# Kernel optimization log

Measured on AMD Instinct MI355X. Metric: run time of the kernel, lower is better.

Reference implementation:

```python
import jax, jax.numpy as jnp
import numpy as np

EPS_LN = 1e-5

def _layernorm(x, g, b):
    mu = x.mean(-1, keepdims=True)
    var = ((x - mu) ** 2).mean(-1, keepdims=True)
    return (x - mu) / jnp.sqrt(var + EPS_LN) * g + b


def setup_inputs() -> dict:
    key = jax.random.key(0)
    B, N, D, H = 4, 2048, 256, 4
    hid = int(D * 2.0)
    ks = jax.random.split(key, 12)
    x = jax.random.normal(ks[0], (B, N, D), jnp.float32)
    Au = jax.random.uniform(ks[1], (N, N)) < 0.004
    A = jnp.logical_or(Au, Au.T)
    A = A.at[jnp.arange(N), jnp.arange(N)].set(False)
    Af = A.astype(jnp.float32)
    deg = Af.sum(axis=1)
    L = jnp.diag(deg) - Af                      # graph Laplacian (N,N), PSD
    adjacency = Af + jnp.eye(N, dtype=jnp.float32)  # self loops so no empty softmax rows
    s = lambda k, sh, f: jax.random.normal(k, sh, jnp.float32) * f
    sc = 1.0 / np.sqrt(D)
    Wc = s(ks[2], (D, D), sc); bc = jnp.zeros((D,), jnp.float32)
    Wq = s(ks[3], (D, D), sc); Wk = s(ks[4], (D, D), sc); Wv = s(ks[5], (D, D), sc)
    Wo = s(ks[6], (D, D), sc); bo = jnp.zeros((D,), jnp.float32)
    W1 = s(ks[7], (D, hid), sc); b1 = jnp.zeros((hid,), jnp.float32)
    W2 = s(ks[8], (hid, D), 1.0 / np.sqrt(hid)); b2 = jnp.zeros((D,), jnp.float32)
    g1 = jnp.ones((D,), jnp.float32); be1 = jnp.zeros((D,), jnp.float32)
    g2 = jnp.ones((D,), jnp.float32); be2 = jnp.zeros((D,), jnp.float32)
    g3 = jnp.ones((D,), jnp.float32); be3 = jnp.zeros((D,), jnp.float32)
    return dict(x=x, L=L, adjacency=adjacency, Wc=Wc, bc=bc, g1=g1, be1=be1,
                Wq=Wq, Wk=Wk, Wv=Wv, Wo=Wo, bo=bo, g2=g2, be2=be2,
                W1=W1, b1=b1, W2=W2, b2=b2, g3=g3, be3=be3)


def reference(x, L, adjacency, Wc, bc, g1, be1, Wq, Wk, Wv, Wo, bo,
              g2, be2, W1, b1, W2, b2, g3, be3):
    B, N, D = x.shape
    H = 4
    hd = D // H
    # --- LaplacianConv: normalize L to eigenvalues in [-1, 1] ---
    eig = jnp.linalg.eigvalsh(L)               # ascending
    lam_max = eig[-1] + 1e-8
    L_norm = 2.0 * L / lam_max - jnp.eye(N, dtype=L.dtype)
    # per-channel matmul in torch == single propagation L_norm @ x
    xp = jnp.einsum('mn,bnf->bmf', L_norm, x)
    h = xp @ Wc + bc
    h = _layernorm(h, g1, be1)
    h = jax.nn.relu(h)
    x1 = h + x                                  # residual (in_dim == out_dim)
    # --- adjacency-masked multi-head attention ---
    q = (x1 @ Wq).reshape(B, N, H, hd).transpose(0, 2, 1, 3)  # (B,H,N,hd)
    k = (x1 @ Wk).reshape(B, N, H, hd).transpose(0, 2, 1, 3)
    v = (x1 @ Wv).reshape(B, N, H, hd).transpose(0, 2, 1, 3)
    scores = jnp.einsum('bhnd,bhmd->bhnm', q, k) / np.sqrt(hd).astype(np.float32)
    scores = jnp.where(adjacency[None, None] > 0, scores, jnp.float32(-1e9))
    attn = jax.nn.softmax(scores, axis=-1)
    o = jnp.einsum('bhnm,bhmd->bhnd', attn, v)
    o = o.transpose(0, 2, 1, 3).reshape(B, N, D)
    o = o @ Wo + bo
    x2 = _layernorm(x1 + o, g2, be2)
    # --- MLP ---
    m = jax.nn.gelu(x2 @ W1 + b1, approximate=False) @ W2 + b2
    return _layernorm(x2 + m, g3, be3)
```

## Files before the change

### kernel.cpp

```cpp
#include <hip/hip_runtime.h>
#include <math.h>

typedef __bf16 bf16;
typedef bf16 bf16x8 __attribute__((ext_vector_type(8)));
typedef float f32x4 __attribute__((ext_vector_type(4)));

#define LDS_PAD 40
#define SENT 2048
#define LANCZOS_M 14

__global__ __launch_bounds__(256) void k_pre(
    const float* __restrict__ Wc, const float* __restrict__ Wq, const float* __restrict__ Wk,
    const float* __restrict__ Wv, const float* __restrict__ Wo, const float* __restrict__ W1,
    const float* __restrict__ W2, const float* __restrict__ x, const float* __restrict__ adj,
    bf16* __restrict__ WcT, bf16* __restrict__ WqT, bf16* __restrict__ WkT,
    bf16* __restrict__ WvT, bf16* __restrict__ WoT, bf16* __restrict__ W1T,
    bf16* __restrict__ W2T, bf16* __restrict__ xT,
    int* __restrict__ cnt, unsigned short* __restrict__ cols,
    const float* __restrict__ L, bf16* __restrict__ Lb)
{
    __shared__ float tile[32][33];
    int z = blockIdx.z;
    if (z == 11) {
        int flat = blockIdx.y * 16 + blockIdx.x;
        if (flat >= 512) return;
        int row = flat * 4 + (threadIdx.x >> 6);
        int lane = threadIdx.x & 63;
        int base = 0;
        for (int c0 = 0; c0 < 2048; c0 += 64) {
            float a = adj[(long)row * 2048 + c0 + lane];
            unsigned long long m = __ballot(a != 0.0f);
            if (a != 0.0f) {
                int pos = base + __popcll(m & ((1ull << lane) - 1ull));
                if (pos < 64) cols[(long)row * 64 + pos] = (unsigned short)(c0 + lane);
            }
            base += __popcll(m);
        }
        int c = base < 64 ? base : 64;
        if (lane >= c) cols[(long)row * 64 + lane] = (unsigned short)SENT;
        if (lane == 0) cnt[row] = c;
        return;
    }
    if (z >= 12) {
        int colBase = (z - 12) * 512 + blockIdx.x * 32;
        int rowBase = blockIdx.y * 32;
        int tx = threadIdx.x & 31, ty = threadIdx.x >> 5;
#pragma unroll
        for (int j = 0; j < 4; ++j) {
            long idx = (long)(rowBase + ty + 8 * j) * 2048 + colBase + tx;
            Lb[idx] = (bf16)L[idx];
        }
        return;
    }
    const float* src; bf16* dst; int R, C;
    switch (z) {
        case 0: src = Wc; dst = WcT; R = 256; C = 256; break;
        case 1: src = Wq; dst = WqT; R = 256; C = 256; break;
        case 2: src = Wk; dst = WkT; R = 256; C = 256; break;
        case 3: src = Wv; dst = WvT; R = 256; C = 256; break;
        case 4: src = Wo; dst = WoT; R = 256; C = 256; break;
        case 5: src = W1; dst = W1T; R = 256; C = 512; break;
        case 6: src = W2; dst = W2T; R = 512; C = 256; break;
        default: {
            int b = z - 7;
            src = x + (long)b * 2048 * 256; dst = xT + (long)b * 256 * 2048;
            R = 2048; C = 256;
        }
    }
    int c0 = blockIdx.x * 32, r0 = blockIdx.y * 32;
    if (c0 >= C || r0 >= R) return;
    int tx = threadIdx.x & 31, ty = threadIdx.x >> 5;
#pragma unroll
    for (int j = 0; j < 4; ++j)
        tile[ty + 8 * j][tx] = src[(long)(r0 + ty + 8 * j) * C + c0 + tx];
    __syncthreads();
#pragma unroll
    for (int j = 0; j < 4; ++j)
        dst[(long)(c0 + ty + 8 * j) * R + r0 + tx] = (bf16)tile[tx][ty + 8 * j];
}

__global__ __launch_bounds__(1024) void k_main(
    const int* __restrict__ cnt, const unsigned short* __restrict__ cols, float* __restrict__ lamOut,
    const bf16* __restrict__ Lb, const bf16* __restrict__ xT, float* __restrict__ xp0f)
{
    __shared__ float va[2064], vb[2064];
    __shared__ float redf[16], redf2[16];
    __shared__ int   redi[16];
    __shared__ float bcast, bcast2;
    __shared__ float alphaA[LANCZOS_M], betaA[LANCZOS_M];
    __shared__ bf16 As[64 * LDS_PAD];
    __shared__ bf16 Bs[256 * LDS_PAD];

    int t = threadIdx.x;
    if (blockIdx.x != 0) {
        int bx = blockIdx.x - 1;
        int rowBlk = (bx & 31) * 64;
        int z  = (bx >> 5) & 3;
        int ks = bx >> 7;
        long kbase = (long)ks * 1024;
        const bf16* BT = xT + (long)z * 256 * 2048;
        int w = t >> 6, lane = t & 63;
        int q = lane >> 4, l15 = lane & 15;
        int wm = w & 3, wn = w >> 2;

        f32x4 acc[4];
#pragma unroll
        for (int i = 0; i < 4; ++i) acc[i] = (f32x4){0.0f, 0.0f, 0.0f, 0.0f};

        int ar = t >> 4, ac = (t & 15) * 2;
        int br = t >> 2, bc = (t & 3) * 8;
        const bf16* Ap = Lb + (long)(rowBlk + ar) * 2048 + kbase + ac;
        const bf16* Bp = BT + (long)br * 2048 + kbase + bc;
        unsigned rA = *(const unsigned*)Ap;
        uint4    rB = *(const uint4*)Bp;
        for (int kt = 0; kt < 1024; kt += 32) {
            __syncthreads();
            *(unsigned*)&As[ar * LDS_PAD + ac] = rA;
            *(uint4*)&Bs[br * LDS_PAD + bc] = rB;
            __syncthreads();
            if (kt + 32 < 1024) {
                rA = *(const unsigned*)(Ap + kt + 32);
                rB = *(const uint4*)(Bp + kt + 32);
            }
            bf16x8 a = *(const bf16x8*)&As[(wm * 16 + l15) * LDS_PAD + q * 8];
#pragma unroll
            for (int nt = 0; nt < 4; ++nt) {
                bf16x8 b = *(const bf16x8*)&Bs[((wn * 4 + nt) * 16 + l15) * LDS_PAD + q * 8];
                acc[nt] = __builtin_amdgcn_mfma_f32_16x16x32_bf16(a, b, acc[nt], 0, 0, 0);
            }
        }
        long zRow = (long)ks * 8192 + (long)z * 2048 + rowBlk + wm * 16 + q * 4;
#pragma unroll
        for (int nt = 0; nt < 4; ++nt) {
            int col = (wn * 4 + nt) * 16 + l15;
#pragma unroll
            for (int r = 0; r < 4; ++r)
                xp0f[(zRow + r) * 256 + col] = acc[nt][r];
        }
        return;
    }
    int wid = t >> 6, lane = t & 63;
    int r0 = t, r1 = t + 1024;
    int c0 = cnt[r0], c1 = cnt[r1];
    int p0 = (c0 + 7) & ~7, p1 = (c1 + 7) & ~7;

    uint4 cr0[8], cr1[8];
#pragma unroll
    for (int j = 0; j < 8; ++j) {
        cr0[j] = ((const uint4*)(cols + (long)r0 * 64))[j];
        cr1[j] = ((const uint4*)(cols + (long)r1 * 64))[j];
    }

    int md = max(c0, c1);
#pragma unroll
    for (int off = 32; off >= 1; off >>= 1) md = max(md, __shfl_xor(md, off));
    if (lane == 0) redi[wid] = md;
    __syncthreads();
    if (t == 0) {
        int m = 0;
        for (int i = 0; i < 16; ++i) m = max(m, redi[i]);
        bcast = (float)(2 * (m - 1)) + 1.0f;
    }
    for (int i = t; i < 2048; i += 1024) {
        unsigned u = (unsigned)i * 2654435761u;
        u ^= u >> 16; u *= 2246822519u; u ^= u >> 13;
        float mag = 0.5f + (float)((u >> 9) & 1023) * (1.0f / 1024.0f);
        va[i] = (u & 1) ? mag : -mag;
    }
    if (t == 0) { va[SENT] = 0.0f; vb[SENT] = 0.0f; }
    __syncthreads();
    float hiBound = bcast;

    float d0 = va[r0], d1 = va[r1];
    float pz = d0 * d0 + d1 * d1;
#pragma unroll
    for (int off = 32; off >= 1; off >>= 1) pz += __shfl_xor(pz, off);
    if (lane == 0) redf[wid] = pz;
    __syncthreads();
    if (t == 0) { float s = 0; for (int i = 0; i < 16; ++i) s += redf[i]; bcast = s; }
    __syncthreads();
    float sc = rsqrtf(fmaxf(bcast, 1e-30f));
    d0 *= sc; d1 *= sc;
    va[r0] = d0; va[r1] = d1;
    __syncthreads();

    float* cur = va; float* nxt = vb;
    float bp = 0.0f;
    float p0r = 0.0f, p1r = 0.0f;
    for (int it = 0; it < LANCZOS_M; ++it) {
        float sum0 = 0.0f, sum1 = 0.0f;
#pragma unroll
        for (int j = 0; j < 8; ++j)
            if (j * 8 < p0) {
                uint4 q = cr0[j];
                sum0 += cur[q.x & 0xffff] + cur[q.x >> 16] + cur[q.y & 0xffff] + cur[q.y >> 16]
                      + cur[q.z & 0xffff] + cur[q.z >> 16] + cur[q.w & 0xffff] + cur[q.w >> 16];
            }
#pragma unroll
        for (int j = 0; j < 8; ++j)
            if (j * 8 < p1) {
                uint4 q = cr1[j];
                sum1 += cur[q.x & 0xffff] + cur[q.x >> 16] + cur[q.y & 0xffff] + cur[q.y >> 16]
                      + cur[q.z & 0xffff] + cur[q.z >> 16] + cur[q.w & 0xffff] + cur[q.w >> 16];
            }
        float u0 = (float)c0 * d0 - sum0 - bp * p0r;
        float u1 = (float)c1 * d1 - sum1 - bp * p1r;
        float puv = u0 * d0 + u1 * d1;
        float puu = u0 * u0 + u1 * u1;
#pragma unroll
        for (int off = 32; off >= 1; off >>= 1) {
            puv += __shfl_xor(puv, off);
            puu += __shfl_xor(puu, off);
        }
        if (lane == 0) { redf[wid] = puv; redf2[wid] = puu; }
        __syncthreads();
        if (t == 0) {
            float sv = 0, su = 0;
            for (int i = 0; i < 16; ++i) { sv += redf[i]; su += redf2[i]; }
            float b = sqrtf(fmaxf(su - sv * sv, 1e-24f));
            alphaA[it] = sv; betaA[it] = b;
            bcast = sv; bcast2 = b;
        }
        __syncthreads();
        float alpha = bcast, beta = bcast2;
        float invb = 1.0f / beta;
        float w0 = u0 - alpha * d0, w1 = u1 - alpha * d1;
        p0r = d0; p1r = d1;
        d0 = w0 * invb; d1 = w1 * invb;
        nxt[r0] = d0; nxt[r1] = d1;
        __syncthreads();
        bp = beta;
        float* tmp = cur; cur = nxt; nxt = tmp;
    }

    if (t < 64) {
        float aa[LANCZOS_M], b2[LANCZOS_M];
#pragma unroll
        for (int i = 0; i < LANCZOS_M; ++i) { aa[i] = alphaA[i]; b2[i] = betaA[i] * betaA[i]; }
        float lo = 0.0f, hi = hiBound;
        for (int round = 0; round < 4; ++round) {
            float step = (hi - lo) * (1.0f / 65.0f);
            float xm = lo + step * (float)(lane + 1);
            float dd = aa[0] - xm;
            int neg = dd < 0.0f ? 1 : 0;
#pragma unroll
            for (int i = 1; i < LANCZOS_M; ++i) {
                float ad = fmaxf(fabsf(dd), 1e-12f);
                dd = (dd < 0.0f) ? -ad : ad;
                dd = aa[i] - xm - b2[i - 1] / dd;
                neg += dd < 0.0f ? 1 : 0;
            }
            unsigned long long mb = __ballot(neg >= LANCZOS_M);
            if (mb == 0ull) {
                lo = lo + step * 64.0f;
            } else {
                int fl = (int)(__ffsll((long long)mb) - 1);
                hi = lo + step * (float)(fl + 1);
                lo = lo + step * (float)fl;
            }
        }
        if (lane == 0) lamOut[0] = 0.5f * (lo + hi) + 1e-8f;
    }
}

template <int TA, int EPI>
__global__ __launch_bounds__(256) void k_gemm(
    const bf16* __restrict__ A0, const float* __restrict__ Apa, const float* __restrict__ Apb,
    const float* __restrict__ Aaux, const bf16* __restrict__ BTg,
    float* __restrict__ outF, bf16* __restrict__ outB,
    const float* __restrict__ bias, const float* __restrict__ resid,
    const float* __restrict__ gam, const float* __restrict__ bet,
    const float* __restrict__ lamPtr,
    int K, long aZ, long btZ, long outZrows, int ldOut)
{
    __shared__ bf16 As[64 * LDS_PAD];
    __shared__ bf16 Bs[256 * LDS_PAD];

    int tid = threadIdx.x;
    int w = tid >> 6, lane = tid & 63;
    int q = lane >> 4, l15 = lane & 15;
    int rowBlk = blockIdx.x * 64;
    int colB = blockIdx.y * 256;
    const bf16* BT = BTg + (long)blockIdx.z * btZ + (long)blockIdx.y * 256 * (long)K;

    float s2 = 0.0f;
    if (TA == 2) s2 = 2.0f / lamPtr[0];

    f32x4 acc[16];
#pragma unroll
    for (int i = 0; i < 16; ++i) acc[i] = (f32x4){0.0f, 0.0f, 0.0f, 0.0f};

    int ar = tid >> 2, ac = (tid & 3) * 8;
    long abase = (long)(rowBlk + ar) * K + ac;
    const bf16* A = A0 + (long)blockIdx.z * aZ;
    const bf16* Bp = BT + (long)tid * K;

    uint4 aR;
    float4 pa0, pa1, pb0, pb1, xa0, xa1;
    uint4 bR0, bR1, bR2, bR3;
    if (TA == 1) {
        aR = *(const uint4*)(A + abase);
    } else {
        pa0 = *(const float4*)(Apa + abase);  pa1 = *(const float4*)(Apa + abase + 4);
        pb0 = *(const float4*)(Apb + abase);  pb1 = *(const float4*)(Apb + abase + 4);
        xa0 = *(const float4*)(Aaux + abase); xa1 = *(const float4*)(Aaux + abase + 4);
    }
    bR0 = ((const uint4*)Bp)[0]; bR1 = ((const uint4*)Bp)[1];
    bR2 = ((const uint4*)Bp)[2]; bR3 = ((const uint4*)Bp)[3];

    for (int kt = 0; kt < K; kt += 32) {
        __syncthreads();
        if (TA == 1) {
            *(uint4*)&As[ar * LDS_PAD + ac] = aR;
        } else {
            float pa[8] = {pa0.x, pa0.y, pa0.z, pa0.w, pa1.x, pa1.y, pa1.z, pa1.w};
            float pb[8] = {pb0.x, pb0.y, pb0.z, pb0.w, pb1.x, pb1.y, pb1.z, pb1.w};
            float xa[8] = {xa0.x, xa0.y, xa0.z, xa0.w, xa1.x, xa1.y, xa1.z, xa1.w};
            union { bf16 h[8]; uint4 u; } pk;
#pragma unroll
            for (int j = 0; j < 8; ++j) pk.h[j] = (bf16)(s2 * (pa[j] + pb[j]) - xa[j]);
            *(uint4*)&As[ar * LDS_PAD + ac] = pk.u;
        }
        {
            bf16* d = &Bs[tid * LDS_PAD];
            *(uint4*)(d + 0)  = bR0;
            *(uint4*)(d + 8)  = bR1;
            *(uint4*)(d + 16) = bR2;
            *(uint4*)(d + 24) = bR3;
        }
        __syncthreads();
        if (kt + 32 < K) {
            long nb = abase + kt + 32;
            if (TA == 1) {
                aR = *(const uint4*)(A + nb);
            } else {
                pa0 = *(const float4*)(Apa + nb);  pa1 = *(const float4*)(Apa + nb + 4);
                pb0 = *(const float4*)(Apb + nb);  pb1 = *(const float4*)(Apb + nb + 4);
                xa0 = *(const float4*)(Aaux + nb); xa1 = *(const float4*)(Aaux + nb + 4);
            }
            const bf16* p = Bp + kt + 32;
            bR0 = ((const uint4*)p)[0]; bR1 = ((const uint4*)p)[1];
            bR2 = ((const uint4*)p)[2]; bR3 = ((const uint4*)p)[3];
        }
        bf16x8 a = *(const bf16x8*)&As[(w * 16 + l15) * LDS_PAD + q * 8];
#pragma unroll
        for (int nt = 0; nt < 16; ++nt) {
            bf16x8 b = *(const bf16x8*)&Bs[(nt * 16 + l15) * LDS_PAD + q * 8];
            acc[nt] = __builtin_amdgcn_mfma_f32_16x16x32_bf16(a, b, acc[nt], 0, 0, 0);
        }
    }

    long zRow = (long)blockIdx.z * outZrows + rowBlk + w * 16 + q * 4;

    if (EPI == 0) {
#pragma unroll
        for (int nt = 0; nt < 16; ++nt) {
            int col = colB + nt * 16 + l15;
#pragma unroll
            for (int r = 0; r < 4; ++r)
                outB[(zRow + r) * (long)ldOut + col] = (bf16)acc[nt][r];
        }
        return;
    }
    if (EPI == 3) {
#pragma unroll
        for (int nt = 0; nt < 16; ++nt) {
            int col = colB + nt * 16 + l15;
            float bi = bias[col];
#pragma unroll
            for (int r = 0; r < 4; ++r) {
                float v = acc[nt][r] + bi;
                float g = 0.5f * v * (1.0f + erff(v * 0.70710678118654752440f));
                outB[(zRow + r) * (long)ldOut + col] = (bf16)g;
            }
        }
        return;
    }
    float s[4] = {0, 0, 0, 0}, sq[4] = {0, 0, 0, 0};
#pragma unroll
    for (int nt = 0; nt < 16; ++nt) {
        int col = colB + nt * 16 + l15;
        float bi = bias[col];
#pragma unroll
        for (int r = 0; r < 4; ++r) {
            float v = acc[nt][r] + bi;
            if (EPI == 2) v += resid[(zRow + r) * 256 + col];
            acc[nt][r] = v;
            s[r] += v; sq[r] += v * v;
        }
    }
#pragma unroll
    for (int off = 1; off <= 8; off <<= 1) {
#pragma unroll
        for (int r = 0; r < 4; ++r) { s[r] += __shfl_xor(s[r], off); sq[r] += __shfl_xor(sq[r], off); }
    }
    float mean[4], rstd[4];
#pragma unroll
    for (int r = 0; r < 4; ++r) {
        mean[r] = s[r] * (1.0f / 256.0f);
        float var = sq[r] * (1.0f / 256.0f) - mean[r] * mean[r];
        rstd[r] = rsqrtf(var + 1e-5f);
    }
#pragma unroll
    for (int nt = 0; nt < 16; ++nt) {
        int col = colB + nt * 16 + l15;
        float gc = gam[col], bc2 = bet[col];
#pragma unroll
        for (int r = 0; r < 4; ++r) {
            float v = (acc[nt][r] - mean[r]) * rstd[r] * gc + bc2;
            if (EPI == 1) v = fmaxf(v, 0.0f) + resid[(zRow + r) * 256 + col];
            long oi = (zRow + r) * (long)ldOut + col;
            outF[oi] = v;
            if (outB) outB[oi] = (bf16)v;
        }
    }
}

__global__ __launch_bounds__(256) void k_attn(const bf16* __restrict__ qg, const bf16* __restrict__ kg,
                                              const bf16* __restrict__ vg, bf16* __restrict__ og,
                                              const int* __restrict__ cnt, const unsigned short* __restrict__ cols)
{
    __shared__ unsigned short sc[64];
    __shared__ float sp[4][64];
    int row = blockIdx.x;
    int b = row >> 11, i = row & 2047;
    int tid = threadIdx.x, h = tid >> 6, lane = tid & 63;
    int c = cnt[i];
    if (tid < 64) sc[tid] = cols[(long)i * 64 + tid];
    __syncthreads();
    long qoff = (long)row * 256 + h * 64 + lane;
    float qd = (float)qg[qoff];
    long kvBase = (long)b * 2048;
    for (int j = 0; j < c; ++j) {
        int col = sc[j];
        float kd = (float)kg[(kvBase + col) * 256 + h * 64 + lane];
        float p = qd * kd;
#pragma unroll
        for (int off = 32; off >= 1; off >>= 1) p += __shfl_xor(p, off);
        if (lane == 0) sp[h][j] = p * 0.125f;
    }
    __syncthreads();
    float sj = (lane < c) ? sp[h][lane] : -3.0e38f;
    float mx = sj;
#pragma unroll
    for (int off = 32; off >= 1; off >>= 1) mx = fmaxf(mx, __shfl_xor(mx, off));
    float e = (lane < c) ? __expf(sj - mx) : 0.0f;
    float ssum = e;
#pragma unroll
    for (int off = 32; off >= 1; off >>= 1) ssum += __shfl_xor(ssum, off);
    if (lane < c) sp[h][lane] = e / ssum;
    __syncthreads();
    float acc = 0.0f;
    for (int j = 0; j < c; ++j) {
        int col = sc[j];
        acc += sp[h][j] * (float)vg[(kvBase + col) * 256 + h * 64 + lane];
    }
    og[qoff] = (bf16)acc;
}

extern "C" void kernel_launch(void* const* d_in, const int* in_sizes, int n_in,
                              void* d_out, int out_size, void* d_ws, size_t ws_size,
                              hipStream_t stream)
{
    const float* x   = (const float*)d_in[0];
    const float* L   = (const float*)d_in[1];
    const float* adj = (const float*)d_in[2];
    const float* Wc  = (const float*)d_in[3];
    const float* bc  = (const float*)d_in[4];
    const float* g1  = (const float*)d_in[5];
    const float* be1 = (const float*)d_in[6];
    const float* Wq  = (const float*)d_in[7];
    const float* Wk  = (const float*)d_in[8];
    const float* Wv  = (const float*)d_in[9];
    const float* Wo  = (const float*)d_in[10];
    const float* bo  = (const float*)d_in[11];
    const float* g2  = (const float*)d_in[12];
    const float* be2 = (const float*)d_in[13];
    const float* W1  = (const float*)d_in[14];
    const float* b1  = (const float*)d_in[15];
    const float* W2  = (const float*)d_in[16];
    const float* b2  = (const float*)d_in[17];
    const float* g3  = (const float*)d_in[18];
    const float* be3 = (const float*)d_in[19];
    float* out = (float*)d_out;

    char* ws = (char*)d_ws;
    size_t off = 0;
    auto alloc = [&](size_t bytes) -> void* {
        void* p = ws + off;
        off = (off + bytes + 255) & ~(size_t)255;
        return p;
    };
    float* lam           = (float*)alloc(256);
    int* cnt             = (int*)alloc(2048 * 4);
    unsigned short* cols = (unsigned short*)alloc(2048 * 64 * 2);
    bf16* WcT = (bf16*)alloc(65536 * 2);
    bf16* WqT = (bf16*)alloc(65536 * 2);
    bf16* WkT = (bf16*)alloc(65536 * 2);
    bf16* WvT = (bf16*)alloc(65536 * 2);
    bf16* WoT = (bf16*)alloc(65536 * 2);
    bf16* W1T = (bf16*)alloc(131072 * 2);
    bf16* W2T = (bf16*)alloc(131072 * 2);
    bf16* Lb  = (bf16*)alloc((size_t)2048 * 2048 * 2);
    bf16* xT  = (bf16*)alloc((size_t)4 * 256 * 2048 * 2);
    float* xp0f = (float*)alloc((size_t)2 * 8192 * 256 * 4);
    float* x1f = (float*)alloc((size_t)8192 * 256 * 4);
    bf16* x1b  = (bf16*)alloc((size_t)8192 * 256 * 2);
    bf16* qb   = (bf16*)alloc((size_t)3 * 8192 * 256 * 2);
    bf16* ob   = (bf16*)alloc((size_t)8192 * 256 * 2);
    float* x2f = (float*)alloc((size_t)8192 * 256 * 4);
    bf16* x2b  = (bf16*)alloc((size_t)8192 * 256 * 2);
    bf16* m1   = (bf16*)alloc((size_t)8192 * 512 * 2);
    (void)in_sizes; (void)n_in; (void)out_size; (void)ws_size;

    dim3 blk(256);
    k_pre<<<dim3(16, 64, 16), blk, 0, stream>>>(Wc, Wq, Wk, Wv, Wo, W1, W2, x, adj,
                                                WcT, WqT, WkT, WvT, WoT, W1T, W2T, xT, cnt, cols,
                                                L, Lb);
    k_main<<<dim3(257), dim3(1024), 0, stream>>>(cnt, cols, lam, Lb, xT, xp0f);
    k_gemm<2, 1><<<dim3(128, 1, 1), blk, 0, stream>>>(
        nullptr, xp0f, xp0f + (size_t)8192 * 256, x, WcT, x1f, x1b, bc, x, g1, be1, lam,
        256, 0L, 0L, 0L, 256);
    k_gemm<1, 0><<<dim3(128, 1, 3), blk, 0, stream>>>(
        x1b, nullptr, nullptr, nullptr, WqT, nullptr, qb, nullptr, nullptr, nullptr, nullptr, nullptr,
        256, 0L, 65536L, 8192L, 256);
    bf16* kb  = qb + (size_t)8192 * 256;
    bf16* vb2 = qb + (size_t)2 * 8192 * 256;
    k_attn<<<dim3(8192), blk, 0, stream>>>(qb, kb, vb2, ob, cnt, cols);
    k_gemm<1, 2><<<dim3(128, 1, 1), blk, 0, stream>>>(
        ob, nullptr, nullptr, nullptr, WoT, x2f, x2b, bo, x1f, g2, be2, nullptr,
        256, 0L, 0L, 0L, 256);
    k_gemm<1, 3><<<dim3(128, 2, 1), blk, 0, stream>>>(
        x2b, nullptr, nullptr, nullptr, W1T, nullptr, m1, b1, nullptr, nullptr, nullptr, nullptr,
        256, 0L, 0L, 0L, 512);
    k_gemm<1, 2><<<dim3(128, 1, 1), blk, 0, stream>>>(
        m1, nullptr, nullptr, nullptr, W2T, out, nullptr, b2, x2f, g3, be3, nullptr,
        512, 0L, 0L, 0L, 256);
}
```

Baseline: 397.3 us.

## Reduce Lanczos barriers via redundant per-wave reductions and unnormalized vector storage

Restructures the Lanczos loop in the eigenvalue-bound block so each iteration needs only one __syncthreads. Every wave now redundantly reduces the per-wave partials itself, with double-buffered reduction slots, instead of thread 0 reducing and broadcasting through shared memory. The unnormalized vector u is stored, and the normalized product is recovered algebraically from the previous alpha and beta. The setup reductions for max degree and initial norm are merged into one barrier. This shortens the serial latency chain of the single Lanczos block, at some risk to numerical behaviour from the recurrence-based normalization.

```diff
diff --git a/kernel.cpp b/kernel.cpp
--- a/kernel.cpp
+++ b/kernel.cpp
@@ -84,10 +84,9 @@
     const bf16* __restrict__ Lb, const bf16* __restrict__ xT, float* __restrict__ xp0f)
 {
     __shared__ float va[2064], vb[2064];
-    __shared__ float redf[16], redf2[16];
+    __shared__ float redf[2][16], redf2[2][16];
     __shared__ int   redi[16];
-    __shared__ float bcast, bcast2;
-    __shared__ float alphaA[LANCZOS_M], betaA[LANCZOS_M];
+    __shared__ float aT[16], bT[16];
     __shared__ bf16 As[64 * LDS_PAD];
     __shared__ bf16 Bs[256 * LDS_PAD];
 
@@ -151,60 +150,63 @@
         cr1[j] = ((const uint4*)(cols + (long)r1 * 64))[j];
     }
 
-    int md = max(c0, c1);
-#pragma unroll
-    for (int off = 32; off >= 1; off >>= 1) md = max(md, __shfl_xor(md, off));
-    if (lane == 0) redi[wid] = md;
-    __syncthreads();
-    if (t == 0) {
-        int m = 0;
-        for (int i = 0; i < 16; ++i) m = max(m, redi[i]);
-        bcast = (float)(2 * (m - 1)) + 1.0f;
-    }
+    float d0raw = 0.0f, d1raw = 0.0f;
     for (int i = t; i < 2048; i += 1024) {
         unsigned u = (unsigned)i * 2654435761u;
         u ^= u >> 16; u *= 2246822519u; u ^= u >> 13;
         float mag = 0.5f + (float)((u >> 9) & 1023) * (1.0f / 1024.0f);
-        va[i] = (u & 1) ? mag : -mag;
+        float v = (u & 1) ? mag : -mag;
+        va[i] = v;
+        if (i == r0) d0raw = v; else d1raw = v;
     }
     if (t == 0) { va[SENT] = 0.0f; vb[SENT] = 0.0f; }
+
+    int md = max(c0, c1);
+#pragma unroll
+    for (int off = 32; off >= 1; off >>= 1) md = max(md, __shfl_xor(md, off));
+    float pz = d0raw * d0raw + d1raw * d1raw;
+#pragma unroll
+    for (int off = 32; off >= 1; off >>= 1) pz += __shfl_xor(pz, off);
+    if (lane == 0) { redi[wid] = md; redf[0][wid] = pz; }
     __syncthreads();
-    float hiBound = bcast;
-
-    float d0 = va[r0], d1 = va[r1];
-    float pz = d0 * d0 + d1 * d1;
-#pragma unroll
-    for (int off = 32; off >= 1; off >>= 1) pz += __shfl_xor(pz, off);
-    if (lane == 0) redf[wid] = pz;
-    __syncthreads();
-    if (t == 0) { float s = 0; for (int i = 0; i < 16; ++i) s += redf[i]; bcast = s; }
-    __syncthreads();
-    float sc = rsqrtf(fmaxf(bcast, 1e-30f));
-    d0 *= sc; d1 *= sc;
-    va[r0] = d0; va[r1] = d1;
-    __syncthreads();
+    int hl = lane & 15;
+    int mm = redi[hl];
+    float nv = redf[0][hl];
+#pragma unroll
+    for (int off = 1; off <= 8; off <<= 1) {
+        mm = max(mm, __shfl_xor(mm, off));
+        nv += __shfl_xor(nv, off);
+    }
+    float g = (float)(2 * (mm - 1)) + 1.0f;
+    float s0 = rsqrtf(fmaxf(nv, 1e-30f));
+    float d0 = d0raw * s0, d1 = d1raw * s0;
 
     float* cur = va; float* nxt = vb;
-    float bp = 0.0f;
-    float p0r = 0.0f, p1r = 0.0f;
+    float bp = 0.0f, p0r = 0.0f, p1r = 0.0f;
+    float Sv0 = 0.0f, Sv1 = 0.0f;
+    float aprev = 0.0f, invbp = 0.0f;
     for (int it = 0; it < LANCZOS_M; ++it) {
-        float sum0 = 0.0f, sum1 = 0.0f;
+        float U0 = 0.0f, U1 = 0.0f;
 #pragma unroll
         for (int j = 0; j < 8; ++j)
             if (j * 8 < p0) {
                 uint4 q = cr0[j];
-                sum0 += cur[q.x & 0xffff] + cur[q.x >> 16] + cur[q.y & 0xffff] + cur[q.y >> 16]
-                      + cur[q.z & 0xffff] + cur[q.z >> 16] + cur[q.w & 0xffff] + cur[q.w >> 16];
+                U0 += cur[q.x & 0xffff] + cur[q.x >> 16] + cur[q.y & 0xffff] + cur[q.y >> 16]
+                    + cur[q.z & 0xffff] + cur[q.z >> 16] + cur[q.w & 0xffff] + cur[q.w >> 16];
             }
 #pragma unroll
         for (int j = 0; j < 8; ++j)
             if (j * 8 < p1) {
                 uint4 q = cr1[j];
-                sum1 += cur[q.x & 0xffff] + cur[q.x >> 16] + cur[q.y & 0xffff] + cur[q.y >> 16]
-                      + cur[q.z & 0xffff] + cur[q.z >> 16] + cur[q.w & 0xffff] + cur[q.w >> 16];
-            }
-        float u0 = (float)c0 * d0 - sum0 - bp * p0r;
-        float u1 = (float)c1 * d1 - sum1 - bp * p1r;
+                U1 += cur[q.x & 0xffff] + cur[q.x >> 16] + cur[q.y & 0xffff] + cur[q.y >> 16]
+                    + cur[q.z & 0xffff] + cur[q.z >> 16] + cur[q.w & 0xffff] + cur[q.w >> 16];
+            }
+        float SvN0, SvN1;
+        if (it == 0) { SvN0 = U0 * s0;                    SvN1 = U1 * s0; }
+        else         { SvN0 = (U0 - aprev * Sv0) * invbp; SvN1 = (U1 - aprev * Sv1) * invbp; }
+        float u0 = (float)c0 * d0 - SvN0 - bp * p0r;
+        float u1 = (float)c1 * d1 - SvN1 - bp * p1r;
+        nxt[r0] = u0; nxt[r1] = u1;
         float puv = u0 * d0 + u1 * d1;
         float puu = u0 * u0 + u1 * u1;
 #pragma unroll
@@ -212,32 +214,32 @@
             puv += __shfl_xor(puv, off);
             puu += __shfl_xor(puu, off);
         }
-        if (lane == 0) { redf[wid] = puv; redf2[wid] = puu; }
+        int par = (it + 1) & 1;
+        if (lane == 0) { redf[par][wid] = puv; redf2[par][wid] = puu; }
         __syncthreads();
-        if (t == 0) {
-            float sv = 0, su = 0;
-            for (int i = 0; i < 16; ++i) { sv += redf[i]; su += redf2[i]; }
-            float b = sqrtf(fmaxf(su - sv * sv, 1e-24f));
-            alphaA[it] = sv; betaA[it] = b;
-            bcast = sv; bcast2 = b;
-        }
-        __syncthreads();
-        float alpha = bcast, beta = bcast2;
+        float pr = (lane < 32) ? redf[par][hl] : redf2[par][hl];
+#pragma unroll
+        for (int off = 1; off <= 8; off <<= 1) pr += __shfl_xor(pr, off);
+        float other = __shfl_xor(pr, 32);
+        float sv = (lane < 32) ? pr : other;
+        float su = (lane < 32) ? other : pr;
+        float alpha = sv;
+        float beta = sqrtf(fmaxf(su - sv * sv, 1e-24f));
         float invb = 1.0f / beta;
+        if (t == 0) { aT[it] = alpha; bT[it] = beta; }
         float w0 = u0 - alpha * d0, w1 = u1 - alpha * d1;
         p0r = d0; p1r = d1;
         d0 = w0 * invb; d1 = w1 * invb;
-        nxt[r0] = d0; nxt[r1] = d1;
-        __syncthreads();
-        bp = beta;
+        Sv0 = SvN0; Sv1 = SvN1;
+        aprev = alpha; invbp = invb; bp = beta;
         float* tmp = cur; cur = nxt; nxt = tmp;
     }
 
-    if (t < 64) {
+    if (wid == 0) {
         float aa[LANCZOS_M], b2[LANCZOS_M];
 #pragma unroll
-        for (int i = 0; i < LANCZOS_M; ++i) { aa[i] = alphaA[i]; b2[i] = betaA[i] * betaA[i]; }
-        float lo = 0.0f, hi = hiBound;
+        for (int i = 0; i < LANCZOS_M; ++i) { aa[i] = aT[i]; b2[i] = bT[i] * bT[i]; }
+        float lo = 0.0f, hi = g;
         for (int round = 0; round < 4; ++round) {
             float step = (hi - lo) * (1.0f / 65.0f);
             float xm = lo + step * (float)(lane + 1);
```

Measured after the change: 436.2 us. +9.8%, slower.

## Fuse L bf16 conversion into propagation GEMM and overlap Wc GEMMs with Lanczos

Applied to the files above, without the earlier changes.

Drops the separate pass that converts L to bf16 and instead converts fp32 L in registers inside the L@x GEMM. Because (2L/λ - I)x·Wc = (2/λ)(Lx)Wc - xWc, the Wc GEMM is split into two λ-independent GEMMs. These run as extra blocks of the Lanczos kernel: the x·Wc blocks start at once, and the (Lx)·Wc blocks spin on an atomic flag until all propagation blocks finish. A small new kernel then applies the λ scale, bias, LayerNorm, ReLU and residual. Lanczos iterations also drop from 14 to 12, and the spin-wait adds a deadlock risk if the waiting blocks become resident before the producer blocks.

```diff
diff --git a/kernel.cpp b/kernel.cpp
--- a/kernel.cpp
+++ b/kernel.cpp
@@ -7,17 +7,16 @@
 
 #define LDS_PAD 40
 #define SENT 2048
-#define LANCZOS_M 14
-
-__global__ __launch_bounds__(256) void k_pre(
+#define LANCZOS_M 12
+
+__global__ __launch_bounds__(256) void k_prep(
     const float* __restrict__ Wc, const float* __restrict__ Wq, const float* __restrict__ Wk,
     const float* __restrict__ Wv, const float* __restrict__ Wo, const float* __restrict__ W1,
     const float* __restrict__ W2, const float* __restrict__ x, const float* __restrict__ adj,
     bf16* __restrict__ WcT, bf16* __restrict__ WqT, bf16* __restrict__ WkT,
     bf16* __restrict__ WvT, bf16* __restrict__ WoT, bf16* __restrict__ W1T,
     bf16* __restrict__ W2T, bf16* __restrict__ xT,
-    int* __restrict__ cnt, unsigned short* __restrict__ cols,
-    const float* __restrict__ L, bf16* __restrict__ Lb)
+    int* __restrict__ cnt, unsigned short* __restrict__ cols)
 {
     __shared__ float tile[32][33];
     int z = blockIdx.z;
@@ -41,17 +40,6 @@
         if (lane == 0) cnt[row] = c;
         return;
     }
-    if (z >= 12) {
-        int colBase = (z - 12) * 512 + blockIdx.x * 32;
-        int rowBase = blockIdx.y * 32;
-        int tx = threadIdx.x & 31, ty = threadIdx.x >> 5;
-#pragma unroll
-        for (int j = 0; j < 4; ++j) {
-            long idx = (long)(rowBase + ty + 8 * j) * 2048 + colBase + tx;
-            Lb[idx] = (bf16)L[idx];
-        }
-        return;
-    }
     const float* src; bf16* dst; int R, C;
     switch (z) {
         case 0: src = Wc; dst = WcT; R = 256; C = 256; break;
@@ -81,7 +69,9 @@
 
 __global__ __launch_bounds__(1024) void k_main(
     const int* __restrict__ cnt, const unsigned short* __restrict__ cols, float* __restrict__ lamOut,
-    const bf16* __restrict__ Lb, const bf16* __restrict__ xT, float* __restrict__ xp0f)
+    const float* __restrict__ L, const bf16* __restrict__ xT, float* __restrict__ xp0f,
+    const bf16* __restrict__ WcT, const float* __restrict__ xg,
+    float* __restrict__ g1o, float* __restrict__ g0o, int* __restrict__ flag)
 {
     __shared__ float va[2064], vb[2064];
     __shared__ float redf[16], redf2[16];
@@ -92,6 +82,65 @@
     __shared__ bf16 Bs[256 * LDS_PAD];
 
     int t = threadIdx.x;
+    int w = t >> 6, lane = t & 63;
+    int q = lane >> 4, l15 = lane & 15;
+    int wm = w & 3, wn = w >> 2;
+
+    if (blockIdx.x >= 257) {
+        bool isG1 = blockIdx.x < 385;
+        int gb = blockIdx.x - (isG1 ? 257 : 385);
+        int rowBlk = gb * 64;
+        if (isG1) {
+            if (t == 0) {
+                while (__hip_atomic_load(flag, __ATOMIC_ACQUIRE, __HIP_MEMORY_SCOPE_AGENT) < 256)
+                    __builtin_amdgcn_s_sleep(2);
+            }
+            __syncthreads();
+        }
+        f32x4 acc[4];
+#pragma unroll
+        for (int i = 0; i < 4; ++i) acc[i] = (f32x4){0.0f, 0.0f, 0.0f, 0.0f};
+        int ar = t >> 4, ac = (t & 15) * 2;
+        int br = t >> 2, bc = (t & 3) * 8;
+        const float* A0 = isG1 ? xp0f : xg;
+        const float* A1 = isG1 ? (xp0f + (long)8192 * 256) : xg;
+        long abase = (long)(rowBlk + ar) * 256 + ac;
+        const bf16* Bp = WcT + br * 256 + bc;
+        float2 fa = *(const float2*)(A0 + abase);
+        float2 fb = isG1 ? *(const float2*)(A1 + abase) : (float2){0.0f, 0.0f};
+        uint4 rB = *(const uint4*)Bp;
+        for (int kt = 0; kt < 256; kt += 32) {
+            __syncthreads();
+            {
+                union { bf16 h[2]; unsigned u; } pk;
+                pk.h[0] = (bf16)(fa.x + fb.x); pk.h[1] = (bf16)(fa.y + fb.y);
+                *(unsigned*)&As[ar * LDS_PAD + ac] = pk.u;
+            }
+            *(uint4*)&Bs[br * LDS_PAD + bc] = rB;
+            __syncthreads();
+            if (kt + 32 < 256) {
+                fa = *(const float2*)(A0 + abase + kt + 32);
+                if (isG1) fb = *(const float2*)(A1 + abase + kt + 32);
+                rB = *(const uint4*)(Bp + kt + 32);
+            }
+            bf16x8 a = *(const bf16x8*)&As[(wm * 16 + l15) * LDS_PAD + q * 8];
+#pragma unroll
+            for (int nt = 0; nt < 4; ++nt) {
+                bf16x8 b = *(const bf16x8*)&Bs[((wn * 4 + nt) * 16 + l15) * LDS_PAD + q * 8];
+                acc[nt] = __builtin_amdgcn_mfma_f32_16x16x32_bf16(a, b, acc[nt], 0, 0, 0);
+            }
+        }
+        float* og = isG1 ? g1o : g0o;
+        long zRow = (long)rowBlk + wm * 16 + q * 4;
+#pragma unroll
+        for (int nt = 0; nt < 4; ++nt) {
+            int col = (wn * 4 + nt) * 16 + l15;
+#pragma unroll
+            for (int r = 0; r < 4; ++r)
+                og[(zRow + r) * 256 + col] = acc[nt][r];
+        }
+        return;
+    }
     if (blockIdx.x != 0) {
         int bx = blockIdx.x - 1;
         int rowBlk = (bx & 31) * 64;
@@ -99,9 +148,6 @@
         int ks = bx >> 7;
         long kbase = (long)ks * 1024;
         const bf16* BT = xT + (long)z * 256 * 2048;
-        int w = t >> 6, lane = t & 63;
-        int q = lane >> 4, l15 = lane & 15;
-        int wm = w & 3, wn = w >> 2;
 
         f32x4 acc[4];
 #pragma unroll
@@ -109,17 +155,21 @@
 
         int ar = t >> 4, ac = (t & 15) * 2;
         int br = t >> 2, bc = (t & 3) * 8;
-        const bf16* Ap = Lb + (long)(rowBlk + ar) * 2048 + kbase + ac;
+        const float* Ap = L + (long)(rowBlk + ar) * 2048 + kbase + ac;
         const bf16* Bp = BT + (long)br * 2048 + kbase + bc;
-        unsigned rA = *(const unsigned*)Ap;
-        uint4    rB = *(const uint4*)Bp;
+        float2 fA = *(const float2*)Ap;
+        uint4  rB = *(const uint4*)Bp;
         for (int kt = 0; kt < 1024; kt += 32) {
             __syncthreads();
-            *(unsigned*)&As[ar * LDS_PAD + ac] = rA;
+            {
+                union { bf16 h[2]; unsigned u; } pk;
+                pk.h[0] = (bf16)fA.x; pk.h[1] = (bf16)fA.y;
+                *(unsigned*)&As[ar * LDS_PAD + ac] = pk.u;
+            }
             *(uint4*)&Bs[br * LDS_PAD + bc] = rB;
             __syncthreads();
             if (kt + 32 < 1024) {
-                rA = *(const unsigned*)(Ap + kt + 32);
+                fA = *(const float2*)(Ap + kt + 32);
                 rB = *(const uint4*)(Bp + kt + 32);
             }
             bf16x8 a = *(const bf16x8*)&As[(wm * 16 + l15) * LDS_PAD + q * 8];
@@ -137,9 +187,12 @@
             for (int r = 0; r < 4; ++r)
                 xp0f[(zRow + r) * 256 + col] = acc[nt][r];
         }
+        __threadfence();
+        __syncthreads();
+        if (t == 0) __hip_atomic_fetch_add(flag, 1, __ATOMIC_RELEASE, __HIP_MEMORY_SCOPE_AGENT);
         return;
     }
-    int wid = t >> 6, lane = t & 63;
+    int wid = w;
     int r0 = t, r1 = t + 1024;
     int c0 = cnt[r0], c1 = cnt[r1];
     int p0 = (c0 + 7) & ~7, p1 = (c1 + 7) & ~7;
@@ -192,16 +245,16 @@
 #pragma unroll
         for (int j = 0; j < 8; ++j)
             if (j * 8 < p0) {
-                uint4 q = cr0[j];
-                sum0 += cur[q.x & 0xffff] + cur[q.x >> 16] + cur[q.y & 0xffff] + cur[q.y >> 16]
-                      + cur[q.z & 0xffff] + cur[q.z >> 16] + cur[q.w & 0xffff] + cur[q.w >> 16];
+                uint4 qq = cr0[j];
+                sum0 += cur[qq.x & 0xffff] + cur[qq.x >> 16] + cur[qq.y & 0xffff] + cur[qq.y >> 16]
+                      + cur[qq.z & 0xffff] + cur[qq.z >> 16] + cur[qq.w & 0xffff] + cur[qq.w >> 16];
             }
 #pragma unroll
         for (int j = 0; j < 8; ++j)
             if (j * 8 < p1) {
-                uint4 q = cr1[j];
-                sum1 += cur[q.x & 0xffff] + cur[q.x >> 16] + cur[q.y & 0xffff] + cur[q.y >> 16]
-                      + cur[q.z & 0xffff] + cur[q.z >> 16] + cur[q.w & 0xffff] + cur[q.w >> 16];
+                uint4 qq = cr1[j];
+                sum1 += cur[qq.x & 0xffff] + cur[qq.x >> 16] + cur[qq.y & 0xffff] + cur[qq.y >> 16]
+                      + cur[qq.z & 0xffff] + cur[qq.z >> 16] + cur[qq.w & 0xffff] + cur[qq.w >> 16];
             }
         float u0 = (float)c0 * d0 - sum0 - bp * p0r;
         float u1 = (float)c1 * d1 - sum1 - bp * p1r;
@@ -233,7 +286,7 @@
         float* tmp = cur; cur = nxt; nxt = tmp;
     }
 
-    if (t < 64) {
+    if (wid == 0) {
         float aa[LANCZOS_M], b2[LANCZOS_M];
 #pragma unroll
         for (int i = 0; i < LANCZOS_M; ++i) { aa[i] = alphaA[i]; b2[i] = betaA[i] * betaA[i]; }
@@ -263,14 +316,46 @@
     }
 }
 
-template <int TA, int EPI>
+__global__ __launch_bounds__(256) void k_x1(
+    const float* __restrict__ g1o, const float* __restrict__ g0o, const float* __restrict__ xg,
+    const float* __restrict__ bc, const float* __restrict__ gam, const float* __restrict__ bet,
+    const float* __restrict__ lamPtr, float* __restrict__ x1f, bf16* __restrict__ x1b)
+{
+    int w = threadIdx.x >> 6, lane = threadIdx.x & 63;
+    long row = (long)blockIdx.x * 4 + w;
+    long base = row * 256 + lane * 4;
+    float s2 = 2.0f / lamPtr[0];
+    float4 a = *(const float4*)(g1o + base);
+    float4 b = *(const float4*)(g0o + base);
+    float4 xv = *(const float4*)(xg + base);
+    float4 bcv = *(const float4*)(bc + lane * 4);
+    float h[4] = { s2 * a.x - b.x + bcv.x, s2 * a.y - b.y + bcv.y,
+                   s2 * a.z - b.z + bcv.z, s2 * a.w - b.w + bcv.w };
+    float s = h[0] + h[1] + h[2] + h[3];
+    float sq = h[0] * h[0] + h[1] * h[1] + h[2] * h[2] + h[3] * h[3];
+#pragma unroll
+    for (int off = 32; off >= 1; off >>= 1) { s += __shfl_xor(s, off); sq += __shfl_xor(sq, off); }
+    float mean = s * (1.0f / 256.0f);
+    float var = sq * (1.0f / 256.0f) - mean * mean;
+    float rstd = rsqrtf(var + 1e-5f);
+    float4 gv = *(const float4*)(gam + lane * 4);
+    float4 bev = *(const float4*)(bet + lane * 4);
+    float o0 = fmaxf((h[0] - mean) * rstd * gv.x + bev.x, 0.0f) + xv.x;
+    float o1 = fmaxf((h[1] - mean) * rstd * gv.y + bev.y, 0.0f) + xv.y;
+    float o2 = fmaxf((h[2] - mean) * rstd * gv.z + bev.z, 0.0f) + xv.z;
+    float o3 = fmaxf((h[3] - mean) * rstd * gv.w + bev.w, 0.0f) + xv.w;
+    *(float4*)(x1f + base) = (float4){o0, o1, o2, o3};
+    union { bf16 h4[4]; uint2 u; } pk;
+    pk.h4[0] = (bf16)o0; pk.h4[1] = (bf16)o1; pk.h4[2] = (bf16)o2; pk.h4[3] = (bf16)o3;
+    *(uint2*)(x1b + base) = pk.u;
+}
+
+template <int EPI>
 __global__ __launch_bounds__(256) void k_gemm(
-    const bf16* __restrict__ A0, const float* __restrict__ Apa, const float* __restrict__ Apb,
-    const float* __restrict__ Aaux, const bf16* __restrict__ BTg,
+    const bf16* __restrict__ A0, const bf16* __restrict__ BTg,
     float* __restrict__ outF, bf16* __restrict__ outB,
     const float* __restrict__ bias, const float* __restrict__ resid,
     const float* __restrict__ gam, const float* __restrict__ bet,
-    const float* __restrict__ lamPtr,
     int K, long aZ, long btZ, long outZrows, int ldOut)
 {
     __shared__ bf16 As[64 * LDS_PAD];
@@ -283,9 +368,6 @@
     int colB = blockIdx.y * 256;
     const bf16* BT = BTg + (long)blockIdx.z * btZ + (long)blockIdx.y * 256 * (long)K;
 
-    float s2 = 0.0f;
-    if (TA == 2) s2 = 2.0f / lamPtr[0];
-
     f32x4 acc[16];
 #pragma unroll
     for (int i = 0; i < 16; ++i) acc[i] = (f32x4){0.0f, 0.0f, 0.0f, 0.0f};
@@ -295,32 +377,13 @@
     const bf16* A = A0 + (long)blockIdx.z * aZ;
     const bf16* Bp = BT + (long)tid * K;
 
-    uint4 aR;
-    float4 pa0, pa1, pb0, pb1, xa0, xa1;
-    uint4 bR0, bR1, bR2, bR3;
-    if (TA == 1) {
-        aR = *(const uint4*)(A + abase);
-    } else {
-        pa0 = *(const float4*)(Apa + abase);  pa1 = *(const float4*)(Apa + abase + 4);
-        pb0 = *(const float4*)(Apb + abase);  pb1 = *(const float4*)(Apb + abase + 4);
-        xa0 = *(const float4*)(Aaux + abase); xa1 = *(const float4*)(Aaux + abase + 4);
-    }
-    bR0 = ((const uint4*)Bp)[0]; bR1 = ((const uint4*)Bp)[1];
-    bR2 = ((const uint4*)Bp)[2]; bR3 = ((const uint4*)Bp)[3];
+    uint4 aR = *(const uint4*)(A + abase);
+    uint4 bR0 = ((const uint4*)Bp)[0], bR1 = ((const uint4*)Bp)[1];
+    uint4 bR2 = ((const uint4*)Bp)[2], bR3 = ((const uint4*)Bp)[3];
 
     for (int kt = 0; kt < K; kt += 32) {
         __syncthreads();
-        if (TA == 1) {
-            *(uint4*)&As[ar * LDS_PAD + ac] = aR;
-        } else {
-            float pa[8] = {pa0.x, pa0.y, pa0.z, pa0.w, pa1.x, pa1.y, pa1.z, pa1.w};
-            float pb[8] = {pb0.x, pb0.y, pb0.z, pb0.w, pb1.x, pb1.y, pb1.z, pb1.w};
-            float xa[8] = {xa0.x, xa0.y, xa0.z, xa0.w, xa1.x, xa1.y, xa1.z, xa1.w};
-            union { bf16 h[8]; uint4 u; } pk;
-#pragma unroll
-            for (int j = 0; j < 8; ++j) pk.h[j] = (bf16)(s2 * (pa[j] + pb[j]) - xa[j]);
-            *(uint4*)&As[ar * LDS_PAD + ac] = pk.u;
-        }
+        *(uint4*)&As[ar * LDS_PAD + ac] = aR;
         {
             bf16* d = &Bs[tid * LDS_PAD];
             *(uint4*)(d + 0)  = bR0;
@@ -330,14 +393,7 @@
         }
         __syncthreads();
         if (kt + 32 < K) {
-            long nb = abase + kt + 32;
-            if (TA == 1) {
-                aR = *(const uint4*)(A + nb);
-            } else {
-                pa0 = *(const float4*)(Apa + nb);  pa1 = *(const float4*)(Apa + nb + 4);
-                pb0 = *(const float4*)(Apb + nb);  pb1 = *(const float4*)(Apb + nb + 4);
-                xa0 = *(const float4*)(Aaux + nb); xa1 = *(const float4*)(Aaux + nb + 4);
-            }
+            aR = *(const uint4*)(A + abase + kt + 32);
             const bf16* p = Bp + kt + 32;
             bR0 = ((const uint4*)p)[0]; bR1 = ((const uint4*)p)[1];
             bR2 = ((const uint4*)p)[2]; bR3 = ((const uint4*)p)[3];
@@ -383,8 +439,7 @@
         float bi = bias[col];
 #pragma unroll
         for (int r = 0; r < 4; ++r) {
-            float v = acc[nt][r] + bi;
-            if (EPI == 2) v += resid[(zRow + r) * 256 + col];
+            float v = acc[nt][r] + bi + resid[(zRow + r) * 256 + col];
             acc[nt][r] = v;
             s[r] += v; sq[r] += v * v;
         }
@@ -408,7 +463,6 @@
 #pragma unroll
         for (int r = 0; r < 4; ++r) {
             float v = (acc[nt][r] - mean[r]) * rstd[r] * gc + bc2;
-            if (EPI == 1) v = fmaxf(v, 0.0f) + resid[(zRow + r) * 256 + col];
             long oi = (zRow + r) * (long)ldOut + col;
             outF[oi] = v;
             if (outB) outB[oi] = (bf16)v;
@@ -492,6 +546,7 @@
         return p;
     };
     float* lam           = (float*)alloc(256);
+    int* flag            = (int*)alloc(256);
     int* cnt             = (int*)alloc(2048 * 4);
     unsigned short* cols = (unsigned short*)alloc(2048 * 64 * 2);
     bf16* WcT = (bf16*)alloc(65536 * 2);
@@ -501,9 +556,10 @@
     bf16* WoT = (bf16*)alloc(65536 * 2);
     bf16* W1T = (bf16*)alloc(131072 * 2);
     bf16* W2T = (bf16*)alloc(131072 * 2);
-    bf16* Lb  = (bf16*)alloc((size_t)2048 * 2048 * 2);
     bf16* xT  = (bf16*)alloc((size_t)4 * 256 * 2048 * 2);
     float* xp0f = (float*)alloc((size_t)2 * 8192 * 256 * 4);
+    float* g1o  = (float*)alloc((size_t)8192 * 256 * 4);
+    float* g0o  = (float*)alloc((size_t)8192 * 256 * 4);
     float* x1f = (float*)alloc((size_t)8192 * 256 * 4);
     bf16* x1b  = (bf16*)alloc((size_t)8192 * 256 * 2);
     bf16* qb   = (bf16*)alloc((size_t)3 * 8192 * 256 * 2);
@@ -513,27 +569,27 @@
     bf16* m1   = (bf16*)alloc((size_t)8192 * 512 * 2);
     (void)in_sizes; (void)n_in; (void)out_size; (void)ws_size;
 
+    hipMemsetAsync(flag, 0, 256, stream);
+
     dim3 blk(256);
-    k_pre<<<dim3(16, 64, 16), blk, 0, stream>>>(Wc, Wq, Wk, Wv, Wo, W1, W2, x, adj,
-                                                WcT, WqT, WkT, WvT, WoT, W1T, W2T, xT, cnt, cols,
-                                                L, Lb);
-    k_main<<<dim3(257), dim3(1024), 0, stream>>>(cnt, cols, lam, Lb, xT, xp0f);
-    k_gemm<2, 1><<<dim3(128, 1, 1), blk, 0, stream>>>(
-        nullptr, xp0f, xp0f + (size_t)8192 * 256, x, WcT, x1f, x1b, bc, x, g1, be1, lam,
-        256, 0L, 0L, 0L, 256);
-    k_gemm<1, 0><<<dim3(128, 1, 3), blk, 0, stream>>>(
-        x1b, nullptr, nullptr, nullptr, WqT, nullptr, qb, nullptr, nullptr, nullptr, nullptr, nullptr,
+    k_prep<<<dim3(16, 64, 12), blk, 0, stream>>>(Wc, Wq, Wk, Wv, Wo, W1, W2, x, adj,
+                                                 WcT, WqT, WkT, WvT, WoT, W1T, W2T, xT, cnt, cols);
+    k_main<<<dim3(513), dim3(1024), 0, stream>>>(cnt, cols, lam, L, xT, xp0f,
+                                                 WcT, x, g1o, g0o, flag);
+    k_x1<<<dim3(2048), blk, 0, stream>>>(g1o, g0o, x, bc, g1, be1, lam, x1f, x1b);
+    k_gemm<0><<<dim3(128, 1, 3), blk, 0, stream>>>(
+        x1b, WqT, nullptr, qb, nullptr, nullptr, nullptr, nullptr,
         256, 0L, 65536L, 8192L, 256);
     bf16* kb  = qb + (size_t)8192 * 256;
     bf16* vb2 = qb + (size_t)2 * 8192 * 256;
     k_attn<<<dim3(8192), blk, 0, stream>>>(qb, kb, vb2, ob, cnt, cols);
-    k_gemm<1, 2><<<dim3(128, 1, 1), blk, 0, stream>>>(
-        ob, nullptr, nullptr, nullptr, WoT, x2f, x2b, bo, x1f, g2, be2, nullptr,
+    k_gemm<2><<<dim3(128, 1, 1), blk, 0, stream>>>(
+        ob, WoT, x2f, x2b, bo, x1f, g2, be2,
         256, 0L, 0L, 0L, 256);
-    k_gemm<1, 3><<<dim3(128, 2, 1), blk, 0, stream>>>(
-        x2b, nullptr, nullptr, nullptr, W1T, nullptr, m1, b1, nullptr, nullptr, nullptr, nullptr,
+    k_gemm<3><<<dim3(128, 2, 1), blk, 0, stream>>>(
+        x2b, W1T, nullptr, m1, b1, nullptr, nullptr, nullptr,
         256, 0L, 0L, 0L, 512);
-    k_gemm<1, 2><<<dim3(128, 1, 1), blk, 0, stream>>>(
-        m1, nullptr, nullptr, nullptr, W2T, out, nullptr, b2, x2f, g3, be3, nullptr,
+    k_gemm<2><<<dim3(128, 1, 1), blk, 0, stream>>>(
+        m1, W2T, out, nullptr, b2, x2f, g3, be3,
         512, 0L, 0L, 0L, 256);
 }
```

After: 545.4 us. +37.3%, slower.

## Fuse L-to-bf16 conversion into propagation GEMM and cut Lanczos iterations

Applied to the files above, without the earlier changes.

Removes the separate pass in the prep kernel that converted the dense fp32 Laplacian to a bf16 buffer. The propagation GEMM now loads fp32 L directly and converts to bf16 while staging into LDS. This drops one full write and re-read of the 2048x2048 matrix, at the cost of doubling the A-operand global load width inside the GEMM. Separately, the Lanczos iteration count for the max-eigenvalue estimate is reduced from 14 to 12, which shortens the serial eigen path but may loosen the lambda_max accuracy.

```diff
diff --git a/kernel.cpp b/kernel.cpp
--- a/kernel.cpp
+++ b/kernel.cpp
@@ -7,7 +7,7 @@
 
 #define LDS_PAD 40
 #define SENT 2048
-#define LANCZOS_M 14
+#define LANCZOS_M 12
 
 __global__ __launch_bounds__(256) void k_pre(
     const float* __restrict__ Wc, const float* __restrict__ Wq, const float* __restrict__ Wk,
@@ -16,8 +16,7 @@
     bf16* __restrict__ WcT, bf16* __restrict__ WqT, bf16* __restrict__ WkT,
     bf16* __restrict__ WvT, bf16* __restrict__ WoT, bf16* __restrict__ W1T,
     bf16* __restrict__ W2T, bf16* __restrict__ xT,
-    int* __restrict__ cnt, unsigned short* __restrict__ cols,
-    const float* __restrict__ L, bf16* __restrict__ Lb)
+    int* __restrict__ cnt, unsigned short* __restrict__ cols)
 {
     __shared__ float tile[32][33];
     int z = blockIdx.z;
@@ -41,17 +40,6 @@
         if (lane == 0) cnt[row] = c;
         return;
     }
-    if (z >= 12) {
-        int colBase = (z - 12) * 512 + blockIdx.x * 32;
-        int rowBase = blockIdx.y * 32;
-        int tx = threadIdx.x & 31, ty = threadIdx.x >> 5;
-#pragma unroll
-        for (int j = 0; j < 4; ++j) {
-            long idx = (long)(rowBase + ty + 8 * j) * 2048 + colBase + tx;
-            Lb[idx] = (bf16)L[idx];
-        }
-        return;
-    }
     const float* src; bf16* dst; int R, C;
     switch (z) {
         case 0: src = Wc; dst = WcT; R = 256; C = 256; break;
@@ -81,7 +69,7 @@
 
 __global__ __launch_bounds__(1024) void k_main(
     const int* __restrict__ cnt, const unsigned short* __restrict__ cols, float* __restrict__ lamOut,
-    const bf16* __restrict__ Lb, const bf16* __restrict__ xT, float* __restrict__ xp0f)
+    const float* __restrict__ L, const bf16* __restrict__ xT, float* __restrict__ xp0f)
 {
     __shared__ float va[2064], vb[2064];
     __shared__ float redf[16], redf2[16];
@@ -109,17 +97,21 @@
 
         int ar = t >> 4, ac = (t & 15) * 2;
         int br = t >> 2, bc = (t & 3) * 8;
-        const bf16* Ap = Lb + (long)(rowBlk + ar) * 2048 + kbase + ac;
+        const float* Ap = L + (long)(rowBlk + ar) * 2048 + kbase + ac;
         const bf16* Bp = BT + (long)br * 2048 + kbase + bc;
-        unsigned rA = *(const unsigned*)Ap;
-        uint4    rB = *(const uint4*)Bp;
+        float2 fA = *(const float2*)Ap;
+        uint4  rB = *(const uint4*)Bp;
         for (int kt = 0; kt < 1024; kt += 32) {
             __syncthreads();
-            *(unsigned*)&As[ar * LDS_PAD + ac] = rA;
+            {
+                union { bf16 h[2]; unsigned u; } pk;
+                pk.h[0] = (bf16)fA.x; pk.h[1] = (bf16)fA.y;
+                *(unsigned*)&As[ar * LDS_PAD + ac] = pk.u;
+            }
             *(uint4*)&Bs[br * LDS_PAD + bc] = rB;
             __syncthreads();
             if (kt + 32 < 1024) {
-                rA = *(const unsigned*)(Ap + kt + 32);
+                fA = *(const float2*)(Ap + kt + 32);
                 rB = *(const uint4*)(Bp + kt + 32);
             }
             bf16x8 a = *(const bf16x8*)&As[(wm * 16 + l15) * LDS_PAD + q * 8];
@@ -501,7 +493,6 @@
     bf16* WoT = (bf16*)alloc(65536 * 2);
     bf16* W1T = (bf16*)alloc(131072 * 2);
     bf16* W2T = (bf16*)alloc(131072 * 2);
-    bf16* Lb  = (bf16*)alloc((size_t)2048 * 2048 * 2);
     bf16* xT  = (bf16*)alloc((size_t)4 * 256 * 2048 * 2);
     float* xp0f = (float*)alloc((size_t)2 * 8192 * 256 * 4);
     float* x1f = (float*)alloc((size_t)8192 * 256 * 4);
@@ -514,10 +505,9 @@
     (void)in_sizes; (void)n_in; (void)out_size; (void)ws_size;
 
     dim3 blk(256);
-    k_pre<<<dim3(16, 64, 16), blk, 0, stream>>>(Wc, Wq, Wk, Wv, Wo, W1, W2, x, adj,
-                                                WcT, WqT, WkT, WvT, WoT, W1T, W2T, xT, cnt, cols,
-                                                L, Lb);
-    k_main<<<dim3(257), dim3(1024), 0, stream>>>(cnt, cols, lam, Lb, xT, xp0f);
+    k_pre<<<dim3(16, 64, 12), blk, 0, stream>>>(Wc, Wq, Wk, Wv, Wo, W1, W2, x, adj,
+                                                WcT, WqT, WkT, WvT, WoT, W1T, W2T, xT, cnt, cols);
+    k_main<<<dim3(257), dim3(1024), 0, stream>>>(cnt, cols, lam, L, xT, xp0f);
     k_gemm<2, 1><<<dim3(128, 1, 1), blk, 0, stream>>>(
         nullptr, xp0f, xp0f + (size_t)8192 * 256, x, WcT, x1f, x1b, bc, x, g1, be1, lam,
         256, 0L, 0L, 0L, 256);
```

New measurement: 384.7 us. 3.2% less time.
